# Performance work log

Measured on AMD Instinct MI355X. Metric: run time of the kernel, lower is better.

The kernel has to match this reference:

```python
import jax, jax.numpy as jnp
import numpy as np

CHUNK = 64

def _l2norm(x, eps=1e-6):
    return x * jax.lax.rsqrt(jnp.sum(x * x, axis=-1, keepdims=True) + eps)

def _gated_delta_rule(query, key, value, g, beta, chunk_size=CHUNK):
    """Chunked gated delta-rule linear attention (Qwen3.5 GatedDeltaNet).
    query/key: [B,S,H,Dk], value: [B,S,H,Dv], g/beta: [B,S,H]. Returns [B,S,H,Dv]."""
    out_dtype = query.dtype
    # use_qk_l2norm_in_kernel=True
    query = _l2norm(query)
    key = _l2norm(key)
    # -> [B,H,S,D] fp32 (matches torch kernel's internal fp32 math)
    q, k, v = [jnp.transpose(x, (0, 2, 1, 3)).astype(jnp.float32) for x in (query, key, value)]
    gg, b = [jnp.transpose(x, (0, 2, 1)).astype(jnp.float32) for x in (g, beta)]
    B, H, S, Dk = k.shape
    Dv = v.shape[-1]
    C = chunk_size
    pad = (-S) % C  # static
    if pad:
        q = jnp.pad(q, ((0, 0), (0, 0), (0, pad), (0, 0)))
        k = jnp.pad(k, ((0, 0), (0, 0), (0, pad), (0, 0)))
        v = jnp.pad(v, ((0, 0), (0, 0), (0, pad), (0, 0)))
        gg = jnp.pad(gg, ((0, 0), (0, 0), (0, pad)))
        b = jnp.pad(b, ((0, 0), (0, 0), (0, pad)))
    Tlen = S + pad
    N = Tlen // C
    q = q * (Dk ** -0.5)
    v_beta = v * b[..., None]
    k_beta = k * b[..., None]
    rs = lambda x: x.reshape(B, H, N, C, x.shape[-1])
    q, k, v_beta, k_beta = map(rs, (q, k, v_beta, k_beta))
    gc = jnp.cumsum(gg.reshape(B, H, N, C), axis=-1)  # within-chunk cumulative log-decay
    tril = jnp.tril(jnp.ones((C, C), bool))
    strict = jnp.tril(jnp.ones((C, C), bool), -1)
    diff = gc[..., :, None] - gc[..., None, :]  # [B,H,N,C,C]
    decay = jnp.where(tril, jnp.exp(jnp.where(tril, diff, 0.0)), 0.0)
    # UT transform: torch's sequential row loop computes (I + strict_tril(k_beta k^T * decay))^{-1}
    M = jnp.where(strict, jnp.einsum('bhnck,bhndk->bhncd', k_beta, k) * decay, 0.0)
    eye = jnp.eye(C, dtype=jnp.float32)
    Tmat = jax.scipy.linalg.solve_triangular(eye + M, jnp.broadcast_to(eye, M.shape), lower=True)
    v_c = Tmat @ v_beta                                   # [B,H,N,C,Dv]
    k_cum = Tmat @ (k_beta * jnp.exp(gc)[..., None])      # [B,H,N,C,Dk]

    def step(state, inp):
        q_i, k_i, v_i, kc_i, dec_i, g_i = inp  # per-chunk [B,H,C,*]
        attn = jnp.einsum('bhck,bhdk->bhcd', q_i, k_i) * dec_i
        v_new = v_i - kc_i @ state
        out_i = (q_i * jnp.exp(g_i)[..., None]) @ state + attn @ v_new
        g_last = g_i[..., -1]
        kd = k_i * jnp.exp(g_last[..., None] - g_i)[..., None]
        state = state * jnp.exp(g_last)[..., None, None] + jnp.einsum('bhck,bhcv->bhkv', kd, v_new)
        return state, out_i

    mv = lambda x: jnp.moveaxis(x, 2, 0)  # chunk axis leading for scan
    init = jnp.zeros((B, H, Dk, Dv), jnp.float32)
    _, outs = jax.lax.scan(step, init, (mv(q), mv(k), mv(v_c), mv(k_cum), mv(decay), mv(gc)))
    out = jnp.moveaxis(outs, 0, 2).reshape(B, H, Tlen, Dv)[:, :, :S]
    return jnp.transpose(out, (0, 2, 1, 3)).astype(out_dtype)


def setup_inputs() -> dict:
    key = jax.random.key(0)
    ks = jax.random.split(key, 5)
    B, S, H, Dk, Dv = 2, 4096, 16, 128, 128
    q = jax.random.normal(ks[0], (B, S, H, Dk), jnp.float32)
    k = jax.random.normal(ks[1], (B, S, H, Dk), jnp.float32)
    v = jax.random.normal(ks[2], (B, S, H, Dv), jnp.float32)
    # g is log-decay, <= 0 (model computes g = -exp(A_log)*softplus(a + dt_bias))
    g = -jax.random.uniform(ks[3], (B, S, H), jnp.float32)
    beta = jax.random.uniform(ks[4], (B, S, H), jnp.float32)  # ~ sigmoid(b)
    return {"query": q, "key": k, "value": v, "g": g, "beta": beta}


def reference(query, key, value, g, beta):
    return _gated_delta_rule(query, key, value, g, beta)
```

## Files before the change

kernel.cpp:

```cpp
#include <hip/hip_runtime.h>
#include <math.h>


namespace {
constexpr int Bn = 2, Sn = 4096, Hn = 16, DKn = 128, DVn = 128, Cn = 64, Nn = 64;
constexpr int NBH = 32;
constexpr long CHUNK_B = 143360;
}

typedef __attribute__((ext_vector_type(4))) float f32x4;
typedef __attribute__((ext_vector_type(8))) _Float16 f16x8;
typedef __attribute__((ext_vector_type(4))) _Float16 f16x4;

__device__ __forceinline__ void fsplit(float x, _Float16& h, _Float16& l) {
  h = (_Float16)x;
  l = (_Float16)(x - (float)h);
}

__device__ __forceinline__ void gl_lds16(const void* g, void* l) {
  __builtin_amdgcn_global_load_lds(
      (const __attribute__((address_space(1))) void*)g,
      (__attribute__((address_space(3))) void*)l, 16, 0, 0);
}

#define MFMA16(D, A, B) D = __builtin_amdgcn_mfma_f32_16x16x32_f16(A, B, D, 0, 0, 0)

__device__ __forceinline__ int sidx(int r, int dk) {
  return r * 128 + (((dk >> 3) ^ (r & 7)) << 3) + (dk & 7);
}

__global__ __launch_bounds__(512, 1) void gdn_phaseA(
    const float* __restrict__ q, const float* __restrict__ k,
    const float* __restrict__ v, const float* __restrict__ g,
    const float* __restrict__ beta, char* __restrict__ wsb,
    int n0, int ncpp)
{
  __shared__ __align__(16) _Float16 sAh[8192], sAl[8192];
  __shared__ __align__(16) _Float16 sQh[8192], sQl[8192];
  __shared__ __align__(16) float sM[64][68];
  __shared__ __align__(16) float satt[4096];
  __shared__ __align__(16) float sV[64 * 132];
  __shared__ float s_gc[64], s_egc[64], s_inv[64], s_ekd[64], s_beta[64];

  const int t    = threadIdx.x;
  const int lane = t & 63;
  const int w    = t >> 6;
  const int pl  = blockIdx.x;
  const int bhx = pl / ncpp;
  const int nl  = pl % ncpp;
  const int n   = n0 + nl;
  const int hh_ = bhx % Hn;
  const int bb_ = bhx / Hn;
  const long base   = (((long)bb_ * Sn + (long)n * Cn) * Hn + hh_) * DKn;
  const long rowstr = (long)Hn * DKn;
  const long gbase  = ((long)bb_ * Sn + (long)n * Cn) * Hn + hh_;
  const long cb     = (long)pl * CHUNK_B;
  const long gloff  = (long)NBH * ncpp * CHUNK_B;

  #pragma unroll
  for (int i = 0; i < 4; ++i) {
    int idx = t + 512 * i;
    int r = idx >> 5, c4 = (idx & 31) << 2;
    *(f32x4*)&sV[r * 132 + c4] = *(const f32x4*)(v + base + (long)r * rowstr + c4);
  }

  if (t < 64) {
    s_beta[t] = beta[gbase + (long)t * Hn];
    float x = g[gbase + (long)t * Hn];
    #pragma unroll
    for (int s = 1; s < 64; s <<= 1) {
      float y = __shfl_up(x, s, 64);
      if (t >= s) x += y;
    }
    s_gc[t]  = x;
    float eg = expf(x);
    s_egc[t] = eg;
    s_inv[t] = expf(-x);
    float g63 = __shfl(x, 63, 64);
    s_ekd[t] = expf(g63 - x);
    if (t == 63) ((float*)(wsb + gloff))[pl] = eg;
  }

  {
    const int r = t >> 3, sub = t & 7;
    f32x4 ka[4], qa[4];
    #pragma unroll
    for (int i = 0; i < 4; ++i) {
      ka[i] = *(const f32x4*)(k + base + (long)r * rowstr + sub * 16 + 4 * i);
      qa[i] = *(const f32x4*)(q + base + (long)r * rowstr + sub * 16 + 4 * i);
    }
    float sk = 0.f, sq = 0.f;
    #pragma unroll
    for (int i = 0; i < 4; ++i) {
      sk += ka[i][0]*ka[i][0] + ka[i][1]*ka[i][1] + ka[i][2]*ka[i][2] + ka[i][3]*ka[i][3];
      sq += qa[i][0]*qa[i][0] + qa[i][1]*qa[i][1] + qa[i][2]*qa[i][2] + qa[i][3]*qa[i][3];
    }
    sk += __shfl_xor(sk, 1, 64); sk += __shfl_xor(sk, 2, 64); sk += __shfl_xor(sk, 4, 64);
    sq += __shfl_xor(sq, 1, 64); sq += __shfl_xor(sq, 2, 64); sq += __shfl_xor(sq, 4, 64);
    const float rk = rsqrtf(sk + 1e-6f);
    const float rq = rsqrtf(sq + 1e-6f) * 0.08838834764831845f;
    #pragma unroll
    for (int i = 0; i < 4; ++i) {
      const int dk0 = sub * 16 + 4 * i;
      const int go = sidx(r, dk0);
      f16x4 h4, l4, qh4, ql4;
      #pragma unroll
      for (int e = 0; e < 4; ++e) {
        _Float16 h_, l_;
        fsplit(ka[i][e] * rk, h_, l_); h4[e] = h_; l4[e] = l_;
        fsplit(qa[i][e] * rq, h_, l_); qh4[e] = h_; ql4[e] = l_;
      }
      *(f16x4*)&sAh[go] = h4;  *(f16x4*)&sAl[go] = l4;
      *(f16x4*)&sQh[go] = qh4; *(f16x4*)&sQl[go] = ql4;
    }
  }
  __syncthreads();

  {
    const int mt  = w & 3;
    const int tc0 = (w >> 2) * 2;
    const f32x4 zero = {0.f, 0.f, 0.f, 0.f};
    f32x4 mk0 = zero, mk1 = zero, ma0 = zero, ma1 = zero;
    #pragma unroll
    for (int kt = 0; kt < 4; ++kt) {
      const int rA = mt * 16 + (lane & 15);
      const int gA = rA * 128 + (((kt * 4 + (lane >> 4)) ^ (rA & 7)) << 3);
      f16x8 fa_h = *(const f16x8*)&sAh[gA];
      f16x8 fa_l = *(const f16x8*)&sAl[gA];
      #pragma unroll
      for (int j = 0; j < 2; ++j) {
        const int rB = (tc0 + j) * 16 + (lane & 15);
        const int gB = rB * 128 + (((kt * 4 + (lane >> 4)) ^ (rB & 7)) << 3);
        f16x8 fb_h = *(const f16x8*)&sAh[gB];
        f16x8 fb_l = *(const f16x8*)&sAl[gB];
        f16x8 fq_h = *(const f16x8*)&sQh[gB];
        f16x8 fq_l = *(const f16x8*)&sQl[gB];
        if (j == 0) {
          MFMA16(mk0, fa_h, fb_h); MFMA16(mk0, fa_h, fb_l); MFMA16(mk0, fa_l, fb_h);
          MFMA16(ma0, fa_h, fq_h); MFMA16(ma0, fa_h, fq_l); MFMA16(ma0, fa_l, fq_h);
        } else {
          MFMA16(mk1, fa_h, fb_h); MFMA16(mk1, fa_h, fb_l); MFMA16(mk1, fa_l, fb_h);
          MFMA16(ma1, fa_h, fq_h); MFMA16(ma1, fa_h, fq_l); MFMA16(ma1, fa_l, fq_h);
        }
      }
    }
    const int r0 = mt * 16 + (lane >> 4) * 4;
    #pragma unroll
    for (int j = 0; j < 2; ++j) {
      const int scol = (tc0 + j) * 16 + (lane & 15);
      const f32x4 mkv = (j == 0) ? mk0 : mk1;
      const f32x4 mav = (j == 0) ? ma0 : ma1;
      #pragma unroll
      for (int e = 0; e < 4; ++e) {
        const int r = r0 + e;
        sM[r][scol] = (r > scol) ? mkv[e] * s_beta[r] * s_egc[r] * s_inv[scol] : 0.f;
      }
      f32x4 av;
      #pragma unroll
      for (int e = 0; e < 4; ++e) {
        const int d = r0 + e;
        av[e] = (scol >= d) ? mav[e] * s_egc[scol] * s_inv[d] : 0.f;
      }
      *(f32x4*)&satt[scol * 64 + (((r0 >> 2) ^ (scol & 3)) << 2)] = av;
    }
  }
  __syncthreads();

  if (t < 256) {
    float X[64];
    const int j = t;
    if (j < 128) {
      #pragma unroll
      for (int i = 0; i < 64; ++i) {
        const int go = sidx(i, j);
        X[i] = ((float)sAh[go] + (float)sAl[go]) * s_beta[i] * s_egc[i];
      }
    } else {
      const int jj = j - 128;
      #pragma unroll
      for (int i = 0; i < 64; ++i)
        X[i] = sV[i * 132 + jj] * s_beta[i];
    }
    #pragma unroll
    for (int i = 1; i < 64; ++i) {
      float s0 = 0.f, s1 = 0.f, s2 = 0.f, s3 = 0.f;
      int l = 0;
      #pragma unroll
      for (; l + 4 <= i; l += 4) {
        f32x4 m = *(const f32x4*)&sM[i][l];
        s0 += m[0] * X[l];     s1 += m[1] * X[l + 1];
        s2 += m[2] * X[l + 2]; s3 += m[3] * X[l + 3];
      }
      float s = (s0 + s2) + (s1 + s3);
      #pragma unroll
      for (; l < i; ++l) s += sM[i][l] * X[l];
      X[i] -= s;
    }
    if (j < 128) {
      _Float16* KCh = (_Float16*)(wsb + cb);
      _Float16* KCl = (_Float16*)(wsb + cb + 16384);
      #pragma unroll
      for (int c = 0; c < 64; ++c) {
        const int tile = (c >> 4) * 4 + (j >> 5);
        const int ln_  = ((j >> 3) & 3) * 16 + (c & 15);
        const int o = tile * 512 + ln_ * 8 + (j & 7);
        _Float16 h_, l_; fsplit(X[c], h_, l_);
        KCh[o] = h_; KCl[o] = l_;
      }
    } else {
      float* VC = (float*)(wsb + cb + 110592);
      const int jj = j - 128;
      #pragma unroll
      for (int a = 0; a < 16; ++a) {
        f32x4 xx;
        xx[0] = X[4*a]; xx[1] = X[4*a+1]; xx[2] = X[4*a+2]; xx[3] = X[4*a+3];
        const int eo = ((jj >> 4) * 4 + (a >> 2)) * 256 + ((a & 3) * 16 + (jj & 15)) * 4;
        *(f32x4*)&VC[eo] = xx;
      }
    }
  } else {
    const int tt = t - 256;
    {
      _Float16* Hh = (_Float16*)(wsb + cb + 32768);
      _Float16* Ll = (_Float16*)(wsb + cb + 49152);
      #pragma unroll
      for (int i = 0; i < 8; ++i) {
        int o = i * 1024 + tt * 4;
        int tile = o >> 9, ln = (o >> 3) & 63;
        int row = (tile >> 2) * 16 + (ln & 15);
        int k0  = (tile & 3) * 32 + (ln >> 4) * 8 + (o & 7);
        const int go = sidx(row, k0);
        f16x4 qh4 = *(const f16x4*)&sQh[go];
        f16x4 ql4 = *(const f16x4*)&sQl[go];
        const float eg = s_egc[row];
        f16x4 hh, ll;
        #pragma unroll
        for (int r = 0; r < 4; ++r) {
          _Float16 h_, l_;
          fsplit(((float)qh4[r] + (float)ql4[r]) * eg, h_, l_);
          hh[r] = h_; ll[r] = l_;
        }
        *(f16x4*)(Hh + o) = hh; *(f16x4*)(Ll + o) = ll;
      }
    }
    {
      _Float16* Hh = (_Float16*)(wsb + cb + 65536);
      _Float16* Ll = (_Float16*)(wsb + cb + 81920);
      #pragma unroll
      for (int i = 0; i < 8; ++i) {
        int o = i * 1024 + tt * 4;
        int tile = o >> 9, ln = (o >> 3) & 63;
        int row = (tile >> 1) * 16 + (ln & 15);
        int k0  = (tile & 1) * 32 + (ln >> 4) * 8 + (o & 7);
        f16x4 hh, ll;
        #pragma unroll
        for (int r = 0; r < 4; ++r) {
          const int c = k0 + r;
          const int go = sidx(c, row);
          _Float16 h_, l_;
          fsplit(((float)sAh[go] + (float)sAl[go]) * s_ekd[c], h_, l_);
          hh[r] = h_; ll[r] = l_;
        }
        *(f16x4*)(Hh + o) = hh; *(f16x4*)(Ll + o) = ll;
      }
    }
    {
      _Float16* Hh = (_Float16*)(wsb + cb + 98304);
      _Float16* Ll = (_Float16*)(wsb + cb + 104448);
      #pragma unroll
      for (int i = 0; i < 3; ++i) {
        int o = i * 1024 + tt * 4;
        int s = o >> 9, ln = (o >> 3) & 63;
        int mt  = (s < 4) ? s : (s - 2);
        int kt2 = (s < 4) ? 0 : 1;
        int row = mt * 16 + (ln & 15);
        int k0  = kt2 * 32 + (ln >> 4) * 8 + (o & 7);
        f32x4 av = *(const f32x4*)&satt[row * 64 + ((((k0 >> 2) ^ (row & 3))) << 2)];
        f16x4 hh, ll;
        #pragma unroll
        for (int r = 0; r < 4; ++r) {
          _Float16 h_, l_; fsplit(av[r], h_, l_);
          hh[r] = h_; ll[r] = l_;
        }
        *(f16x4*)(Hh + o) = hh; *(f16x4*)(Ll + o) = ll;
      }
    }
  }
}

#define VMW(N) do { asm volatile("s_waitcnt vmcnt(" #N ")" ::: "memory"); \
                    __builtin_amdgcn_sched_barrier(0); } while (0)
#define BAR() do { __builtin_amdgcn_s_barrier(); \
                   __builtin_amdgcn_sched_barrier(0); } while (0)

#define STAGEW2(dst, srcB, nt) do {                                   \
    const char* s_ = (const char*)(srcB);                             \
    char* d_ = (char*)(dst);                                          \
    _Pragma("unroll")                                                 \
    for (int t_ = wave; t_ < (nt); t_ += 2)                           \
      gl_lds16(s_ + t_ * 1024 + lane * 16, d_ + t_ * 1024 + lane * 16); \
  } while (0)

__global__ __launch_bounds__(128, 1) void gdn_phaseB(
    char* __restrict__ wsb, int n0, int ncpp, int lastpass)
{
  __shared__ __align__(16) _Float16 sKCh[8192], sKCl[8192];
  __shared__ __align__(16) _Float16 sQGh[8192], sQGl[8192];
  __shared__ __align__(16) _Float16 sKDh[8192], sKDl[8192];
  __shared__ __align__(16) _Float16 sAT[6144];
  __shared__ __align__(16) _Float16 Sb[2][2][16][128];
  __shared__ __align__(16) _Float16 Ub[2][2][16][64];

  const int tid  = threadIdx.x;
  const int wave = tid >> 6;
  const int lane = tid & 63;
  const int jrow = lane & 15;
  const int kgrp = lane >> 4;
  const int jx3  = (jrow & 7) << 3;

  const int blk    = blockIdx.x;
  const int bhl    = blk & 31;
  const int sharer = blk >> 5;
  const int jb     = sharer * 2 + wave;
  const long gloff = (long)NBH * ncpp * CHUNK_B;
  const float* GLp = (const float*)(wsb + gloff);
  float* STp = (float*)(wsb + gloff + 32768) + (((long)bhl * 8 + jb) * 64 + lane) * 32;
  float* outw = (float*)(wsb + gloff + 32768 + 2097152);
  const char* cbase = wsb + (long)bhl * ncpp * CHUNK_B;

  f32x4 S[8];
  const f32x4 zero = {0.f, 0.f, 0.f, 0.f};
  if (n0 == 0) {
    #pragma unroll
    for (int i = 0; i < 8; ++i) S[i] = zero;
  } else {
    #pragma unroll
    for (int i = 0; i < 8; ++i) S[i] = *(const f32x4*)(STp + i * 4);
  }
  #pragma unroll
  for (int dt = 0; dt < 8; ++dt) {
    f16x4 hh, ll; _Float16 h_, l_;
    #pragma unroll
    for (int r = 0; r < 4; ++r) { fsplit(S[dt][r], h_, l_); hh[r] = h_; ll[r] = l_; }
    const int cx = (dt * 16 + kgrp * 4) ^ jx3;
    *(f16x4*)&Sb[wave][0][jrow][cx] = hh;
    *(f16x4*)&Sb[wave][1][jrow][cx] = ll;
  }

  f32x4 vcv[4];
  {
    const float* VC0 = (const float*)(cbase + 110592);
    #pragma unroll
    for (int ct = 0; ct < 4; ++ct)
      vcv[ct] = *(const f32x4*)(VC0 + ((jb * 4 + ct) * 64 + lane) * 4);
  }
  float glc = GLp[(long)bhl * ncpp];
  STAGEW2(sKCh, cbase +     0, 16); STAGEW2(sKCl, cbase + 16384, 16);
  STAGEW2(sQGh, cbase + 32768, 16); STAGEW2(sQGl, cbase + 49152, 16);
  asm volatile("s_waitcnt vmcnt(0) lgkmcnt(0)" ::: "memory");
  __builtin_amdgcn_sched_barrier(0);
  BAR();

  #pragma unroll 1
  for (int nl = 0; nl < ncpp; ++nl) {
    const int  np  = (nl + 1 < ncpp) ? nl + 1 : nl;
    const char* cbp = cbase + (long)nl * CHUNK_B;
    const char* cbn = cbase + (long)np * CHUNK_B;

    VMW(4); BAR();
    STAGEW2(sKDh, cbp + 65536, 16); STAGEW2(sKDl, cbp + 81920, 16);
    STAGEW2(sAT,  cbp + 98304, 12);
    f32x4 vcvN[4];
    {
      const float* VCn = (const float*)(cbn + 110592);
      #pragma unroll
      for (int ct = 0; ct < 4; ++ct)
        vcvN[ct] = *(const f32x4*)(VCn + ((jb * 4 + ct) * 64 + lane) * 4);
    }
    const float glN = GLp[(long)bhl * ncpp + np];

    f16x8 sbh[4], sbl[4];
    #pragma unroll
    for (int kt = 0; kt < 4; ++kt) {
      const int cx = (kt * 32 + kgrp * 8) ^ jx3;
      sbh[kt] = *(const f16x8*)&Sb[wave][0][jrow][cx];
      sbl[kt] = *(const f16x8*)&Sb[wave][1][jrow][cx];
    }
    f32x4 aA[4], aB[4], aC[4], oA[4], oB[4], oC[4];
    #pragma unroll
    for (int i = 0; i < 4; ++i) {
      aA[i] = zero; aB[i] = zero; aC[i] = zero;
      oA[i] = zero; oB[i] = zero; oC[i] = zero;
    }
    #pragma unroll
    for (int kt = 0; kt < 4; ++kt) {
      #pragma unroll
      for (int mt = 0; mt < 4; ++mt) {
        const int tl = mt * 4 + kt;
        f16x8 ah = *(const f16x8*)&sKCh[tl * 512 + lane * 8];
        f16x8 al = *(const f16x8*)&sKCl[tl * 512 + lane * 8];
        MFMA16(aA[mt], ah, sbh[kt]);
        MFMA16(aB[mt], ah, sbl[kt]);
        MFMA16(aC[mt], al, sbh[kt]);
        f16x8 qh = *(const f16x8*)&sQGh[tl * 512 + lane * 8];
        f16x8 ql = *(const f16x8*)&sQGl[tl * 512 + lane * 8];
        MFMA16(oA[mt], qh, sbh[kt]);
        MFMA16(oB[mt], qh, sbl[kt]);
        MFMA16(oC[mt], ql, sbh[kt]);
      }
    }
    #pragma unroll
    for (int ct = 0; ct < 4; ++ct) {
      f32x4 uu = vcv[ct] - (aA[ct] + aB[ct] + aC[ct]);
      f16x4 hh, ll; _Float16 h_, l_;
      #pragma unroll
      for (int r = 0; r < 4; ++r) { fsplit(uu[r], h_, l_); hh[r] = h_; ll[r] = l_; }
      const int cu = (ct * 16 + kgrp * 4) ^ jx3;
      *(f16x4*)&Ub[wave][0][jrow][cu] = hh;
      *(f16x4*)&Ub[wave][1][jrow][cu] = ll;
    }
    f16x8 ubh[2], ubl[2];
    #pragma unroll
    for (int kt2 = 0; kt2 < 2; ++kt2) {
      const int cx = (kt2 * 32 + kgrp * 8) ^ jx3;
      ubh[kt2] = *(const f16x8*)&Ub[wave][0][jrow][cx];
      ubl[kt2] = *(const f16x8*)&Ub[wave][1][jrow][cx];
    }

    VMW(4); BAR();
    STAGEW2(sKCh, cbn +     0, 16); STAGEW2(sKCl, cbn + 16384, 16);
    STAGEW2(sQGh, cbn + 32768, 16); STAGEW2(sQGl, cbn + 49152, 16);

    #pragma unroll
    for (int kt2 = 0; kt2 < 2; ++kt2) {
      #pragma unroll
      for (int mt = 0; mt < 4; ++mt) {
        if (kt2 == 1 && mt < 2) continue;
        const int slot = (kt2 == 0) ? mt : (mt + 2);
        f16x8 ah = *(const f16x8*)&sAT[slot * 512 + lane * 8];
        f16x8 al = *(const f16x8*)&sAT[3072 + slot * 512 + lane * 8];
        MFMA16(oA[mt], ah, ubh[kt2]);
        MFMA16(oB[mt], ah, ubl[kt2]);
        MFMA16(oC[mt], al, ubh[kt2]);
      }
    }
    {
      float* slab = outw + ((long)(bhl * ncpp + nl) * 8192) + jb * 1024;
      #pragma unroll
      for (int ct = 0; ct < 4; ++ct) {
        f32x4 o4 = oA[ct] + oB[ct] + oC[ct];
        *(f32x4*)(slab + (ct * 64 + lane) * 4) = o4;
      }
    }
    #pragma unroll
    for (int i = 0; i < 8; ++i) {
      S[i][0] *= glc; S[i][1] *= glc; S[i][2] *= glc; S[i][3] *= glc;
    }
    #pragma unroll
    for (int kt2 = 0; kt2 < 2; ++kt2) {
      #pragma unroll
      for (int dt = 0; dt < 8; ++dt) {
        const int tl = dt * 2 + kt2;
        f16x8 ah = *(const f16x8*)&sKDh[tl * 512 + lane * 8];
        f16x8 al = *(const f16x8*)&sKDl[tl * 512 + lane * 8];
        MFMA16(S[dt], ah, ubh[kt2]);
        MFMA16(S[dt], ah, ubl[kt2]);
        MFMA16(S[dt], al, ubh[kt2]);
      }
    }
    #pragma unroll
    for (int dt = 0; dt < 8; ++dt) {
      f16x4 hh, ll; _Float16 h_, l_;
      #pragma unroll
      for (int r = 0; r < 4; ++r) { fsplit(S[dt][r], h_, l_); hh[r] = h_; ll[r] = l_; }
      const int cx = (dt * 16 + kgrp * 4) ^ jx3;
      *(f16x4*)&Sb[wave][0][jrow][cx] = hh;
      *(f16x4*)&Sb[wave][1][jrow][cx] = ll;
    }

    #pragma unroll
    for (int ct = 0; ct < 4; ++ct) vcv[ct] = vcvN[ct];
    glc = glN;
  }

  if (!lastpass) {
    #pragma unroll
    for (int i = 0; i < 8; ++i) *(f32x4*)(STp + i * 4) = S[i];
  }
}

__global__ __launch_bounds__(256, 1) void gdn_epi(
    const char* __restrict__ wsb, float* __restrict__ out,
    int n0, int ncpp)
{
  __shared__ float sT[64][132];
  const int t   = threadIdx.x;
  const int pl  = blockIdx.x;
  const int bhl = pl / ncpp;
  const int nl  = pl % ncpp;
  const int n   = n0 + nl;
  const int h   = bhl % Hn;
  const int b   = bhl / Hn;
  const long gloff = (long)NBH * ncpp * CHUNK_B;
  const float* slab = (const float*)(wsb + gloff + 32768 + 2097152) + (long)pl * 8192;

  #pragma unroll
  for (int i = 0; i < 8; ++i) {
    int idx = t + 256 * i;
    int o = idx * 4;
    int jb = o >> 10, ct = (o >> 8) & 3, ln = (o >> 2) & 63;
    int row = ct * 16 + (ln >> 4) * 4;
    int col = jb * 16 + (ln & 15);
    f32x4 v = *(const f32x4*)(slab + o);
    sT[row + 0][col] = v[0]; sT[row + 1][col] = v[1];
    sT[row + 2][col] = v[2]; sT[row + 3][col] = v[3];
  }
  __syncthreads();
  const long obase = (((long)b * Sn + (long)n * 64) * Hn + h) * DVn;
  #pragma unroll
  for (int i = 0; i < 8; ++i) {
    int idx = t + 256 * i;
    int r2 = idx >> 5, c4 = (idx & 31) << 2;
    *(f32x4*)(out + obase + (long)r2 * (Hn * DVn) + c4) = *(const f32x4*)&sT[r2][c4];
  }
}

extern "C" void kernel_launch(void* const* d_in, const int* in_sizes, int n_in,
                              void* d_out, int out_size, void* d_ws, size_t ws_size,
                              hipStream_t stream) {
  (void)in_sizes; (void)n_in; (void)out_size;
  const float* q    = (const float*)d_in[0];
  const float* k    = (const float*)d_in[1];
  const float* v    = (const float*)d_in[2];
  const float* g    = (const float*)d_in[3];
  const float* beta = (const float*)d_in[4];
  char*  ws  = (char*)d_ws;
  float* out = (float*)d_out;

  int NCP = 8;
  for (int c = 64; c >= 8; c >>= 1) {
    long need = (long)NBH * c * CHUNK_B + 32768 + 2097152
              + (long)NBH * c * 32768;
    if ((size_t)need <= ws_size) { NCP = c; break; }
  }

  for (int n0 = 0; n0 < Nn; n0 += NCP) {
    const int last = (n0 + NCP >= Nn) ? 1 : 0;
    hipLaunchKernelGGL(gdn_phaseA, dim3(NBH * NCP), dim3(512), 0, stream,
                       q, k, v, g, beta, ws, n0, NCP);
    hipLaunchKernelGGL(gdn_phaseB, dim3(128), dim3(128), 0, stream,
                       ws, n0, NCP, last);
    hipLaunchKernelGGL(gdn_epi, dim3(NBH * NCP), dim3(256), 0, stream,
                       ws, out, n0, NCP);
  }
}
```

Baseline: 467.3 us.

## Parallelize chunk recurrence across groups with affine-map scan kernel

Adds a gdn_scan kernel that, for each group of 8 chunks, computes the affine state transition (a matrix A from an identity start and an offset b from a zero start) in parallel. phaseB then runs one block set per group, composes the prior groups' transitions to get its starting state, and processes only its 8 chunks. This turns the long sequential per-head recurrence into parallel work across many more blocks, since phaseB previously launched only 128 blocks. The cost is the extra scan kernel, extra workspace, redundant composition work that grows with group index, a double-buffered state slot, and a cap on NCP at 32.

Result: slower. 626.7 us (+34.1%).

```diff
diff --git a/kernel.cpp b/kernel.cpp
--- a/kernel.cpp
+++ b/kernel.cpp
@@ -6,6 +6,9 @@
 constexpr int Bn = 2, Sn = 4096, Hn = 16, DKn = 128, DVn = 128, Cn = 64, Nn = 64;
 constexpr int NBH = 32;
 constexpr long CHUNK_B = 143360;
+constexpr long ST_SLOT = 2097152;
+constexpr long AG_SZ   = 8388608;
+constexpr long BG_SZ   = 8388608;
 }
 
 typedef __attribute__((ext_vector_type(4))) float f32x4;
@@ -301,8 +304,194 @@
       gl_lds16(s_ + t_ * 1024 + lane * 16, d_ + t_ * 1024 + lane * 16); \
   } while (0)
 
+__global__ __launch_bounds__(128, 1) void gdn_scan(
+    char* __restrict__ wsb, int ncpp, int ng)
+{
+  __shared__ __align__(16) _Float16 sKCh[2][8192], sKCl[2][8192];
+  __shared__ __align__(16) _Float16 sKDh[2][8192], sKDl[2][8192];
+  __shared__ __align__(16) _Float16 Sb[2][2][16][128];
+  __shared__ __align__(16) _Float16 Ub[2][2][16][64];
+
+  const int tid  = threadIdx.x;
+  const int wave = tid >> 6;
+  const int lane = tid & 63;
+  const int jrow = lane & 15;
+  const int kgrp = lane >> 4;
+  const int jx3  = (jrow & 7) << 3;
+
+  const int half  = NBH * ng * 4;
+  const int withb = (blockIdx.x < half) ? 1 : 0;
+  const int bb    = blockIdx.x % half;
+  const int bhl   = bb & 31;
+  const int gs    = bb >> 5;
+  const int sharer = gs & 3;
+  const int grp    = gs >> 2;
+  const int jb     = sharer * 2 + wave;
+
+  const long ARR  = (long)NBH * ncpp * CHUNK_B;
+  const float* GLp = (const float*)(wsb + ARR);
+  const long AGoff = ARR + 32768 + 2 * ST_SLOT;
+  const long BGoff = AGoff + AG_SZ;
+  const char* cbase = wsb + ((long)bhl * ncpp + grp * 8) * CHUNK_B;
+
+  f32x4 S[8];
+  const f32x4 zero = {0.f, 0.f, 0.f, 0.f};
+  if (withb) {
+    #pragma unroll
+    for (int i = 0; i < 8; ++i) S[i] = zero;
+  } else {
+    #pragma unroll
+    for (int dt = 0; dt < 8; ++dt) {
+      #pragma unroll
+      for (int r = 0; r < 4; ++r)
+        S[dt][r] = (dt * 16 + kgrp * 4 + r == jb * 16 + jrow) ? 1.f : 0.f;
+    }
+  }
+  #pragma unroll
+  for (int dt = 0; dt < 8; ++dt) {
+    f16x4 hh, ll; _Float16 h_, l_;
+    #pragma unroll
+    for (int r = 0; r < 4; ++r) { fsplit(S[dt][r], h_, l_); hh[r] = h_; ll[r] = l_; }
+    const int cx = (dt * 16 + kgrp * 4) ^ jx3;
+    *(f16x4*)&Sb[wave][0][jrow][cx] = hh;
+    *(f16x4*)&Sb[wave][1][jrow][cx] = ll;
+  }
+
+  f32x4 vcv[4];
+  if (withb) {
+    const float* VC0 = (const float*)(cbase + 110592);
+    #pragma unroll
+    for (int ct = 0; ct < 4; ++ct)
+      vcv[ct] = *(const f32x4*)(VC0 + ((jb * 4 + ct) * 64 + lane) * 4);
+  }
+  float glc = GLp[(long)bhl * ncpp + grp * 8];
+  STAGEW2(sKCh[0], cbase +     0, 16); STAGEW2(sKCl[0], cbase + 16384, 16);
+  STAGEW2(sKDh[0], cbase + 65536, 16); STAGEW2(sKDl[0], cbase + 81920, 16);
+  asm volatile("s_waitcnt vmcnt(0) lgkmcnt(0)" ::: "memory");
+  __builtin_amdgcn_sched_barrier(0);
+  BAR();
+
+  int cur = 0;
+  f32x4 vcvN[4];
+  float glN = glc;
+  #pragma unroll 1
+  for (int nl2 = 0; nl2 < 8; ++nl2) {
+    if (nl2 > 0) {
+      VMW(0); BAR();
+      cur ^= 1;
+      if (withb) { vcv[0]=vcvN[0]; vcv[1]=vcvN[1]; vcv[2]=vcvN[2]; vcv[3]=vcvN[3]; }
+      glc = glN;
+    }
+    if (nl2 < 7) {
+      const char* cbn = cbase + (long)(nl2 + 1) * CHUNK_B;
+      STAGEW2(sKCh[cur ^ 1], cbn +     0, 16); STAGEW2(sKCl[cur ^ 1], cbn + 16384, 16);
+      STAGEW2(sKDh[cur ^ 1], cbn + 65536, 16); STAGEW2(sKDl[cur ^ 1], cbn + 81920, 16);
+      if (withb) {
+        const float* VCn = (const float*)(cbn + 110592);
+        #pragma unroll
+        for (int ct = 0; ct < 4; ++ct)
+          vcvN[ct] = *(const f32x4*)(VCn + ((jb * 4 + ct) * 64 + lane) * 4);
+      }
+      glN = GLp[(long)bhl * ncpp + grp * 8 + nl2 + 1];
+    }
+
+    f16x8 sbh[4], sbl[4];
+    #pragma unroll
+    for (int kt = 0; kt < 4; ++kt) {
+      const int cx = (kt * 32 + kgrp * 8) ^ jx3;
+      sbh[kt] = *(const f16x8*)&Sb[wave][0][jrow][cx];
+      sbl[kt] = *(const f16x8*)&Sb[wave][1][jrow][cx];
+    }
+    f32x4 aA[4], aB[4], aC[4];
+    #pragma unroll
+    for (int i = 0; i < 4; ++i) { aA[i] = zero; aB[i] = zero; aC[i] = zero; }
+    #pragma unroll
+    for (int kt = 0; kt < 4; ++kt) {
+      #pragma unroll
+      for (int mt = 0; mt < 4; ++mt) {
+        const int tl = mt * 4 + kt;
+        f16x8 ah = *(const f16x8*)&sKCh[cur][tl * 512 + lane * 8];
+        f16x8 al = *(const f16x8*)&sKCl[cur][tl * 512 + lane * 8];
+        MFMA16(aA[mt], ah, sbh[kt]);
+        MFMA16(aB[mt], ah, sbl[kt]);
+        MFMA16(aC[mt], al, sbh[kt]);
+      }
+    }
+    #pragma unroll
+    for (int ct = 0; ct < 4; ++ct) {
+      f32x4 uu = withb ? (vcv[ct] - (aA[ct] + aB[ct] + aC[ct]))
+                       : (zero - (aA[ct] + aB[ct] + aC[ct]));
+      f16x4 hh, ll; _Float16 h_, l_;
+      #pragma unroll
+      for (int r = 0; r < 4; ++r) { fsplit(uu[r], h_, l_); hh[r] = h_; ll[r] = l_; }
+      const int cu = (ct * 16 + kgrp * 4) ^ jx3;
+      *(f16x4*)&Ub[wave][0][jrow][cu] = hh;
+      *(f16x4*)&Ub[wave][1][jrow][cu] = ll;
+    }
+    f16x8 ubh[2], ubl[2];
+    #pragma unroll
+    for (int kt2 = 0; kt2 < 2; ++kt2) {
+      const int cx = (kt2 * 32 + kgrp * 8) ^ jx3;
+      ubh[kt2] = *(const f16x8*)&Ub[wave][0][jrow][cx];
+      ubl[kt2] = *(const f16x8*)&Ub[wave][1][jrow][cx];
+    }
+
+    #pragma unroll
+    for (int i = 0; i < 8; ++i) {
+      S[i][0] *= glc; S[i][1] *= glc; S[i][2] *= glc; S[i][3] *= glc;
+    }
+    #pragma unroll
+    for (int kt2 = 0; kt2 < 2; ++kt2) {
+      #pragma unroll
+      for (int dt = 0; dt < 8; ++dt) {
+        const int tl = dt * 2 + kt2;
+        f16x8 ah = *(const f16x8*)&sKDh[cur][tl * 512 + lane * 8];
+        f16x8 al = *(const f16x8*)&sKDl[cur][tl * 512 + lane * 8];
+        MFMA16(S[dt], ah, ubh[kt2]);
+        MFMA16(S[dt], ah, ubl[kt2]);
+        MFMA16(S[dt], al, ubh[kt2]);
+      }
+    }
+    #pragma unroll
+    for (int dt = 0; dt < 8; ++dt) {
+      f16x4 hh, ll; _Float16 h_, l_;
+      #pragma unroll
+      for (int r = 0; r < 4; ++r) { fsplit(S[dt][r], h_, l_); hh[r] = h_; ll[r] = l_; }
+      const int cx = (dt * 16 + kgrp * 4) ^ jx3;
+      *(f16x4*)&Sb[wave][0][jrow][cx] = hh;
+      *(f16x4*)&Sb[wave][1][jrow][cx] = ll;
+    }
+  }
+
+  if (withb) {
+    float* bgp = (float*)(wsb + BGoff)
+               + (((long)(bhl * ng + grp) * 8 + jb) * 64 + lane) * 32;
+    #pragma unroll
+    for (int i = 0; i < 8; ++i) *(f32x4*)(bgp + i * 4) = S[i];
+  } else {
+    BAR();
+    float* mf = (float*)&sKCh[0][0];
+    #pragma unroll
+    for (int dt = 0; dt < 8; ++dt) {
+      #pragma unroll
+      for (int r = 0; r < 4; ++r)
+        mf[wave * 2176 + (dt * 16 + kgrp * 4 + r) * 17 + jrow] = S[dt][r];
+    }
+    __syncthreads();
+    _Float16* AGh = (_Float16*)(wsb + AGoff + (long)(bhl * ng + grp) * 65536);
+    _Float16* AGl = AGh + 16384;
+    for (int vv = tid; vv < 4096; vv += 128) {
+      const int r = vv >> 5, c = vv & 31;
+      const float val = mf[(c >> 4) * 2176 + r * 17 + (c & 15)];
+      _Float16 h_, l_; fsplit(val, h_, l_);
+      const int off = ((r >> 4) * 4 + sharer) * 512 + ((r & 15) + (c >> 3) * 16) * 8 + (c & 7);
+      AGh[off] = h_; AGl[off] = l_;
+    }
+  }
+}
+
 __global__ __launch_bounds__(128, 1) void gdn_phaseB(
-    char* __restrict__ wsb, int n0, int ncpp, int lastpass)
+    char* __restrict__ wsb, int ncpp, int ng, int pass, int lastpass)
 {
   __shared__ __align__(16) _Float16 sKCh[8192], sKCl[8192];
   __shared__ __align__(16) _Float16 sQGh[8192], sQGl[8192];
@@ -320,22 +509,76 @@
 
   const int blk    = blockIdx.x;
   const int bhl    = blk & 31;
-  const int sharer = blk >> 5;
+  const int gs     = blk >> 5;
+  const int sharer = gs & 3;
+  const int grp    = gs >> 2;
   const int jb     = sharer * 2 + wave;
-  const long gloff = (long)NBH * ncpp * CHUNK_B;
-  const float* GLp = (const float*)(wsb + gloff);
-  float* STp = (float*)(wsb + gloff + 32768) + (((long)bhl * 8 + jb) * 64 + lane) * 32;
-  float* outw = (float*)(wsb + gloff + 32768 + 2097152);
-  const char* cbase = wsb + (long)bhl * ncpp * CHUNK_B;
+
+  const long ARR  = (long)NBH * ncpp * CHUNK_B;
+  const float* GLp = (const float*)(wsb + ARR);
+  const long SToff = ARR + 32768;
+  const long AGoff = SToff + 2 * ST_SLOT;
+  const long BGoff = AGoff + AG_SZ;
+  const long OUToff = BGoff + BG_SZ;
+  const int wslot = pass & 1, rslot = wslot ^ 1;
+  const float* STr = (const float*)(wsb + SToff + (long)rslot * ST_SLOT)
+                   + (((long)bhl * 8 + jb) * 64 + lane) * 32;
+  float* STw = (float*)(wsb + SToff + (long)wslot * ST_SLOT)
+             + (((long)bhl * 8 + jb) * 64 + lane) * 32;
+  float* outw = (float*)(wsb + OUToff);
+  const char* cbase = wsb + ((long)bhl * ncpp + grp * 8) * CHUNK_B;
+
+  STAGEW2(sKCh, cbase +     0, 16); STAGEW2(sKCl, cbase + 16384, 16);
+  STAGEW2(sQGh, cbase + 32768, 16); STAGEW2(sQGl, cbase + 49152, 16);
 
   f32x4 S[8];
   const f32x4 zero = {0.f, 0.f, 0.f, 0.f};
-  if (n0 == 0) {
+  if (pass == 0) {
     #pragma unroll
     for (int i = 0; i < 8; ++i) S[i] = zero;
   } else {
     #pragma unroll
-    for (int i = 0; i < 8; ++i) S[i] = *(const f32x4*)(STp + i * 4);
+    for (int i = 0; i < 8; ++i) S[i] = *(const f32x4*)(STr + i * 4);
+  }
+
+  for (int gg = 0; gg < grp; ++gg) {
+    #pragma unroll
+    for (int dt = 0; dt < 8; ++dt) {
+      f16x4 hh, ll; _Float16 h_, l_;
+      #pragma unroll
+      for (int r = 0; r < 4; ++r) { fsplit(S[dt][r], h_, l_); hh[r] = h_; ll[r] = l_; }
+      const int cx = (dt * 16 + kgrp * 4) ^ jx3;
+      *(f16x4*)&Sb[wave][0][jrow][cx] = hh;
+      *(f16x4*)&Sb[wave][1][jrow][cx] = ll;
+    }
+    f16x8 tbh[4], tbl[4];
+    #pragma unroll
+    for (int kt = 0; kt < 4; ++kt) {
+      const int cx = (kt * 32 + kgrp * 8) ^ jx3;
+      tbh[kt] = *(const f16x8*)&Sb[wave][0][jrow][cx];
+      tbl[kt] = *(const f16x8*)&Sb[wave][1][jrow][cx];
+    }
+    const _Float16* Ah = (const _Float16*)(wsb + AGoff + (long)(bhl * ng + gg) * 65536);
+    const _Float16* Al = Ah + 16384;
+    const float* bgp = (const float*)(wsb + BGoff)
+                     + (((long)(bhl * ng + gg) * 8 + jb) * 64 + lane) * 32;
+    f32x4 acc2[8];
+    #pragma unroll
+    for (int rt = 0; rt < 8; ++rt) acc2[rt] = *(const f32x4*)(bgp + rt * 4);
+    #pragma unroll
+    for (int rt = 0; rt < 8; ++rt) {
+      #pragma unroll
+      for (int kt = 0; kt < 4; ++kt) {
+        const int tl = rt * 4 + kt;
+        f16x8 ah = *(const f16x8*)(Ah + tl * 512 + lane * 8);
+        f16x8 al = *(const f16x8*)(Al + tl * 512 + lane * 8);
+        MFMA16(acc2[rt], ah, tbh[kt]);
+        MFMA16(acc2[rt], ah, tbl[kt]);
+        MFMA16(acc2[rt], al, tbh[kt]);
+      }
+    }
+    #pragma unroll
+    for (int rt = 0; rt < 8; ++rt) S[rt] = acc2[rt];
   }
   #pragma unroll
   for (int dt = 0; dt < 8; ++dt) {
@@ -354,17 +597,15 @@
     for (int ct = 0; ct < 4; ++ct)
       vcv[ct] = *(const f32x4*)(VC0 + ((jb * 4 + ct) * 64 + lane) * 4);
   }
-  float glc = GLp[(long)bhl * ncpp];
-  STAGEW2(sKCh, cbase +     0, 16); STAGEW2(sKCl, cbase + 16384, 16);
-  STAGEW2(sQGh, cbase + 32768, 16); STAGEW2(sQGl, cbase + 49152, 16);
+  float glc = GLp[(long)bhl * ncpp + grp * 8];
   asm volatile("s_waitcnt vmcnt(0) lgkmcnt(0)" ::: "memory");
   __builtin_amdgcn_sched_barrier(0);
   BAR();
 
   #pragma unroll 1
-  for (int nl = 0; nl < ncpp; ++nl) {
-    const int  np  = (nl + 1 < ncpp) ? nl + 1 : nl;
-    const char* cbp = cbase + (long)nl * CHUNK_B;
+  for (int nl2 = 0; nl2 < 8; ++nl2) {
+    const int  np  = (nl2 + 1 < 8) ? nl2 + 1 : nl2;
+    const char* cbp = cbase + (long)nl2 * CHUNK_B;
     const char* cbn = cbase + (long)np * CHUNK_B;
 
     VMW(4); BAR();
@@ -377,7 +618,7 @@
       for (int ct = 0; ct < 4; ++ct)
         vcvN[ct] = *(const f32x4*)(VCn + ((jb * 4 + ct) * 64 + lane) * 4);
     }
-    const float glN = GLp[(long)bhl * ncpp + np];
+    const float glN = GLp[(long)bhl * ncpp + grp * 8 + np];
 
     f16x8 sbh[4], sbl[4];
     #pragma unroll
@@ -445,7 +686,7 @@
       }
     }
     {
-      float* slab = outw + ((long)(bhl * ncpp + nl) * 8192) + jb * 1024;
+      float* slab = outw + ((long)(bhl * ncpp + grp * 8 + nl2) * 8192) + jb * 1024;
       #pragma unroll
       for (int ct = 0; ct < 4; ++ct) {
         f32x4 o4 = oA[ct] + oB[ct] + oC[ct];
@@ -483,9 +724,9 @@
     glc = glN;
   }
 
-  if (!lastpass) {
-    #pragma unroll
-    for (int i = 0; i < 8; ++i) *(f32x4*)(STp + i * 4) = S[i];
+  if (!lastpass && grp == ng - 1) {
+    #pragma unroll
+    for (int i = 0; i < 8; ++i) *(f32x4*)(STw + i * 4) = S[i];
   }
 }
 
@@ -501,8 +742,9 @@
   const int n   = n0 + nl;
   const int h   = bhl % Hn;
   const int b   = bhl / Hn;
-  const long gloff = (long)NBH * ncpp * CHUNK_B;
-  const float* slab = (const float*)(wsb + gloff + 32768 + 2097152) + (long)pl * 8192;
+  const long ARR = (long)NBH * ncpp * CHUNK_B;
+  const long OUToff = ARR + 32768 + 2 * ST_SLOT + AG_SZ + BG_SZ;
+  const float* slab = (const float*)(wsb + OUToff) + (long)pl * 8192;
 
   #pragma unroll
   for (int i = 0; i < 8; ++i) {
@@ -538,18 +780,23 @@
   float* out = (float*)d_out;
 
   int NCP = 8;
-  for (int c = 64; c >= 8; c >>= 1) {
-    long need = (long)NBH * c * CHUNK_B + 32768 + 2097152
+  for (int c = 32; c >= 8; c >>= 1) {
+    long need = (long)NBH * c * CHUNK_B + 32768 + 2 * ST_SLOT + AG_SZ + BG_SZ
               + (long)NBH * c * 32768;
     if ((size_t)need <= ws_size) { NCP = c; break; }
   }
-
-  for (int n0 = 0; n0 < Nn; n0 += NCP) {
+  const int NG = NCP / 8;
+
+  int pass = 0;
+  for (int n0 = 0; n0 < Nn; n0 += NCP, ++pass) {
     const int last = (n0 + NCP >= Nn) ? 1 : 0;
     hipLaunchKernelGGL(gdn_phaseA, dim3(NBH * NCP), dim3(512), 0, stream,
                        q, k, v, g, beta, ws, n0, NCP);
-    hipLaunchKernelGGL(gdn_phaseB, dim3(128), dim3(128), 0, stream,
-                       ws, n0, NCP, last);
+    if (NG > 1)
+      hipLaunchKernelGGL(gdn_scan, dim3(2 * NBH * NG * 4), dim3(128), 0, stream,
+                         ws, NCP, NG);
+    hipLaunchKernelGGL(gdn_phaseB, dim3(NBH * NG * 4), dim3(128), 0, stream,
+                       ws, NCP, NG, pass, last);
     hipLaunchKernelGGL(gdn_epi, dim3(NBH * NCP), dim3(256), 0, stream,
                        ws, out, n0, NCP);
   }
```
